# Kernel tuning notes

Measured on AMD Instinct MI355X. Metric: run time of the kernel, lower is better.

Reference implementation:

```python
import jax, jax.numpy as jnp
import numpy as np

T, B, C, H, L = 384, 48, 256, 256, 2


def setup_inputs() -> dict:
    key = jax.random.key(0)
    ks = jax.random.split(key, 8)
    s = 1.0 / np.sqrt(H)  # torch GRUCell uniform(-1/sqrt(H), 1/sqrt(H)) init
    xav = np.sqrt(2.0 / (H + 1))  # xavier_normal_ for the [1,H] skip-gate linear
    return {
        "x": jax.random.normal(ks[0], (T, B, C), jnp.float32),
        "hiddens": jax.random.normal(ks[1], (L, 1, H), jnp.float32),
        "w_ih": jax.random.uniform(ks[2], (L, 3 * H, C), jnp.float32, -s, s),
        "w_hh": jax.random.uniform(ks[3], (L, 3 * H, H), jnp.float32, -s, s),
        "b_ih": jax.random.uniform(ks[4], (L, 3 * H), jnp.float32, -s, s),
        "b_hh": jax.random.uniform(ks[5], (L, 3 * H), jnp.float32, -s, s),
        "lw": jax.random.normal(ks[6], (L, 1, H), jnp.float32) * xav,
        "lb": jnp.ones((L, 1), jnp.float32),  # linear.bias.data.fill_(1)
    }


def _ste(v):
    # straight-through round: forward round, backward identity
    return v + jax.lax.stop_gradient(jnp.round(v) - v)


def reference(x, hiddens, w_ih, w_hh, b_ih, b_hh, lw, lb):
    Tn, Bn, _ = x.shape
    Ln, _, Hn = hiddens.shape
    skip = jnp.zeros((Bn,), dtype=bool)          # carried across layers (as in torch loop)
    du = jnp.zeros((Bn, 1), x.dtype)             # delta_u, carried across layers
    inp = x
    hs, bus = [], []
    for i in range(Ln):
        wi, wh, bi, bh = w_ih[i], w_hh[i], b_ih[i], b_hh[i]
        lwi, lbi = lw[i], lb[i]
        h0 = jnp.broadcast_to(hiddens[i], (Bn, Hn))  # h.repeat(1, bs, 1)
        u0 = jnp.ones((Bn, 1), x.dtype)              # u reset per layer

        def step(carry, x_t):
            h, u, skp, d = carry
            bu = _ste(u)                                  # [B,1]
            # GRUCell: gates order (r, z, n)
            gi = x_t @ wi.T + bi                          # [B,3H]
            gh = h @ wh.T + bh                            # [B,3H]
            i_r, i_z, i_n = jnp.split(gi, 3, axis=1)
            h_r, h_z, h_n = jnp.split(gh, 3, axis=1)
            r = jax.nn.sigmoid(i_r + h_r)
            z = jax.nn.sigmoid(i_z + h_z)
            n = jnp.tanh(i_n + r * h_n)
            cand = (1.0 - z) * n + z * h
            # non-skip branch
            h_ns = cand * bu
            d_ns = jax.nn.sigmoid(h_ns @ lwi.T + lbi)     # [B,1]
            s = skp[:, None]
            new_h = jnp.where(s, h * (1.0 - bu), h_ns)
            new_d = jnp.where(s, d, d_ns)
            new_u = jnp.where(s, jnp.clip(u + d, 0.0, 1.0) * (1.0 - bu), d_ns * bu)
            # n_skips_after = ceil(0.5/new_u) - 1 ; skip if > 0 (non-diff path)
            nsa = jnp.ceil(0.5 / jax.lax.stop_gradient(new_u)) - 1.0
            new_skip = nsa[:, 0] > 0
            return (new_h, new_u, new_skip, new_d), (new_h, bu)

        (h_f, _, skip, du), (ys, bu_seq) = jax.lax.scan(step, (h0, u0, skip, du), inp)
        inp = ys                 # [T,B,H] feeds next layer
        hs.append(h_f)           # final hidden [B,H]
        bus.append(bu_seq)       # [T,B,1]
    out = inp
    hs = jnp.stack(hs, axis=0)                                   # [L,B,H]
    total_u = jnp.concatenate([b[:, :, 0].T for b in bus], 1)    # [B, L*T]
    return (out, hs, total_u)
```

## Files before the change

kernel.cpp:

```cpp
#include <hip/hip_runtime.h>
#include <stdint.h>


#define T_STEPS 384
#define BATCH   48
#define HID     256

__device__ __forceinline__ float sigm_(float x) { return 1.f / (1.f + __expf(-x)); }
__device__ __forceinline__ float tanh_(float x) {
    float ax = fabsf(x);
    float e  = __expf(-2.f * ax);
    float r  = (1.f - e) / (1.f + e);
    return copysignf(r, x);
}

__global__ __launch_bounds__(256, 2) void gemm_nt(const float* __restrict__ X,
                                                  const float* __restrict__ W,
                                                  const float* __restrict__ B,
                                                  float* __restrict__ O)
{
    __shared__ float As[32 * 140];
    __shared__ float Bs[32 * 68];

    const int tid = threadIdx.x;
    const int tx  = tid & 15;
    const int ty  = tid >> 4;
    const int n0  = blockIdx.x * 64;
    const int m0  = blockIdx.y * 128;

    float acc[8][4];
#pragma unroll
    for (int i = 0; i < 8; ++i)
#pragma unroll
        for (int j = 0; j < 4; ++j) acc[i][j] = 0.f;

    const float4 bias4 = *reinterpret_cast<const float4*>(B + n0 + tx * 4);

    for (int kc = 0; kc < 8; ++kc) {
        const int k0 = kc * 32;
        float4 a[4], bb[2];
#pragma unroll
        for (int j = 0; j < 4; ++j) {
            int f = tid + 256 * j, r = f >> 3, cq = f & 7;
            a[j] = *reinterpret_cast<const float4*>(X + (size_t)(m0 + r) * 256 + k0 + cq * 4);
        }
#pragma unroll
        for (int j = 0; j < 2; ++j) {
            int f = tid + 256 * j, r = f >> 3, cq = f & 7;
            bb[j] = *reinterpret_cast<const float4*>(W + (size_t)(n0 + r) * 256 + k0 + cq * 4);
        }
        __syncthreads();
#pragma unroll
        for (int j = 0; j < 4; ++j) {
            int f = tid + 256 * j, r = f >> 3, cq = f & 7;
            As[(cq * 4 + 0) * 140 + r] = a[j].x;
            As[(cq * 4 + 1) * 140 + r] = a[j].y;
            As[(cq * 4 + 2) * 140 + r] = a[j].z;
            As[(cq * 4 + 3) * 140 + r] = a[j].w;
        }
#pragma unroll
        for (int j = 0; j < 2; ++j) {
            int f = tid + 256 * j, r = f >> 3, cq = f & 7;
            Bs[(cq * 4 + 0) * 68 + r] = bb[j].x;
            Bs[(cq * 4 + 1) * 68 + r] = bb[j].y;
            Bs[(cq * 4 + 2) * 68 + r] = bb[j].z;
            Bs[(cq * 4 + 3) * 68 + r] = bb[j].w;
        }
        __syncthreads();
#pragma unroll 8
        for (int kk = 0; kk < 32; ++kk) {
            float4 av0 = *reinterpret_cast<const float4*>(As + kk * 140 + ty * 8);
            float4 av1 = *reinterpret_cast<const float4*>(As + kk * 140 + ty * 8 + 4);
            float4 bv  = *reinterpret_cast<const float4*>(Bs + kk * 68 + tx * 4);
            float am[8] = {av0.x, av0.y, av0.z, av0.w, av1.x, av1.y, av1.z, av1.w};
            float bn[4] = {bv.x, bv.y, bv.z, bv.w};
#pragma unroll
            for (int i = 0; i < 8; ++i)
#pragma unroll
                for (int j = 0; j < 4; ++j) acc[i][j] = fmaf(am[i], bn[j], acc[i][j]);
        }
    }
#pragma unroll
    for (int i = 0; i < 8; ++i) {
        int row = m0 + ty * 8 + i;
        float4 o;
        o.x = acc[i][0] + bias4.x;
        o.y = acc[i][1] + bias4.y;
        o.z = acc[i][2] + bias4.z;
        o.w = acc[i][3] + bias4.w;
        *reinterpret_cast<float4*>(O + (size_t)row * 768 + n0 + tx * 4) = o;
    }
}

__global__ __launch_bounds__(512, 2) void rec_layer(
    const float* __restrict__ GI, float* __restrict__ Yout,
    const float* __restrict__ whh, const float* __restrict__ bhh,
    const float* __restrict__ lwl, const float* __restrict__ lbl,
    const float* __restrict__ hid,
    unsigned long long* XH, unsigned long long* PD,
    float* __restrict__ hsout, float* __restrict__ tuout)
{
    __shared__ float hbuf[2112];
    __shared__ float pdw[2][8];

    const int tid  = threadIdx.x;
    const int lane = tid & 63;
    const int w    = tid >> 6;
    const int g    = lane & 15;
    const int s    = lane >> 4;
    const int b    = blockIdx.x % 48;
    const int p    = blockIdx.x / 48;
    const int q    = 1 - p;
    const int c    = p * 128 + w * 16 + g;

    float4 Wr[16], Wz[16], Wn[16];
    {
        const float4* wr4 = reinterpret_cast<const float4*>(whh + (size_t)c * 256 + s * 64);
        const float4* wz4 = reinterpret_cast<const float4*>(whh + (size_t)(256 + c) * 256 + s * 64);
        const float4* wn4 = reinterpret_cast<const float4*>(whh + (size_t)(512 + c) * 256 + s * 64);
#pragma unroll
        for (int i = 0; i < 16; ++i) { Wr[i] = wr4[i]; Wz[i] = wz4[i]; Wn[i] = wn4[i]; }
    }

    const float bhr = bhh[c], bhz = bhh[256 + c], bhn = bhh[512 + c];
    const float lwc = lwl[c];
    const float lbv = lbl[0];

    if (tid < 256) {
        float v = hid[tid];
        hbuf[tid] = v; hbuf[264 + tid] = v; hbuf[528 + tid] = v; hbuf[792 + tid] = v;
    }
    __syncthreads();

    float u = 1.f, d = 0.f;
    bool  skip = false;
    int   ns = 0;
    int   hp = 0;

    unsigned long long* XHb = XH + b * 512;
    unsigned long long* PDb = PD + b * 4;

    for (int t = 0; t < T_STEPS; ++t) {
        const float bu  = rintf(u);
        const float obu = 1.f - bu;
        const size_t yrow = ((size_t)t * 48 + b) * 256;

        if (skip) {
            float* hb = hbuf + hp * 1056;
            if (s == 0) {
                float hcv = hb[c];
                float nh  = hcv * obu;
                if (bu != 0.f) { hb[c] = nh; hb[264 + c] = nh; hb[528 + c] = nh; hb[792 + c] = nh; }
                Yout[yrow + c] = nh;
                if (t == T_STEPS - 1) hsout[b * 256 + c] = nh;
            }
            if (p == 0 && tid == 0) tuout[b * 768 + t] = bu;
            u    = fminf(fmaxf(u + d, 0.f), 1.f) * obu;
            skip = (u < 0.5f);
            __syncthreads();
        } else {
            const int sl = ns & 1;
            const unsigned int tag = (unsigned int)ns + 1u;
            const size_t gbase = ((size_t)t * 48 + b) * 768 + c;
            const float gir = GI[gbase], giz = GI[gbase + 256], gin = GI[gbase + 512];

            float ar = 0.f, az = 0.f, an = 0.f;
            const float4* h4 = reinterpret_cast<const float4*>(hbuf + hp * 1056 + s * 328);
#pragma unroll
            for (int i = 0; i < 16; ++i) {
                float4 hv = h4[i];
                ar = fmaf(Wr[i].x, hv.x, ar); ar = fmaf(Wr[i].y, hv.y, ar);
                ar = fmaf(Wr[i].z, hv.z, ar); ar = fmaf(Wr[i].w, hv.w, ar);
                az = fmaf(Wz[i].x, hv.x, az); az = fmaf(Wz[i].y, hv.y, az);
                az = fmaf(Wz[i].z, hv.z, az); az = fmaf(Wz[i].w, hv.w, az);
                an = fmaf(Wn[i].x, hv.x, an); an = fmaf(Wn[i].y, hv.y, an);
                an = fmaf(Wn[i].z, hv.z, an); an = fmaf(Wn[i].w, hv.w, an);
            }
            ar += __shfl_xor(ar, 16); ar += __shfl_xor(ar, 32);
            az += __shfl_xor(az, 16); az += __shfl_xor(az, 32);
            an += __shfl_xor(an, 16); an += __shfl_xor(an, 32);

            float hcv = hbuf[hp * 1056 + s * 264 + c];
            float rr  = sigm_(gir + ar + bhr);
            float zz  = sigm_(giz + az + bhz);
            float nn  = tanh_(gin + rr * (an + bhn));
            float nh  = ((1.f - zz) * nn + zz * hcv) * bu;
            float pdv = nh * lwc;

            float* hbn = hbuf + (hp ^ 1) * 1056;
            if (s == 0) {
                hbn[c] = nh; hbn[264 + c] = nh; hbn[528 + c] = nh; hbn[792 + c] = nh;
                Yout[yrow + c] = nh;
                if (t == T_STEPS - 1) hsout[b * 256 + c] = nh;
                unsigned long long pk = ((unsigned long long)tag << 32) |
                                        (unsigned long long)__float_as_uint(nh);
                __hip_atomic_store(XHb + sl * 256 + c, pk, __ATOMIC_RELAXED, __HIP_MEMORY_SCOPE_AGENT);
            }
            pdv += __shfl_xor(pdv, 1);  pdv += __shfl_xor(pdv, 2);  pdv += __shfl_xor(pdv, 4);
            pdv += __shfl_xor(pdv, 8);  pdv += __shfl_xor(pdv, 16); pdv += __shfl_xor(pdv, 32);
            pdv *= 0.25f;
            if (lane == 0) pdw[sl][w] = pdv;
            if (p == 0 && tid == 0) tuout[b * 768 + t] = bu;
            __syncthreads();

            float ownpd = ((pdw[sl][0] + pdw[sl][1]) + (pdw[sl][2] + pdw[sl][3]))
                        + ((pdw[sl][4] + pdw[sl][5]) + (pdw[sl][6] + pdw[sl][7]));
            if (tid == 0) {
                unsigned long long pk = ((unsigned long long)tag << 32) |
                                        (unsigned long long)__float_as_uint(ownpd);
                __hip_atomic_store(PDb + sl * 2 + p, pk, __ATOMIC_RELAXED, __HIP_MEMORY_SCOPE_AGENT);
            }
            if (tid < 128) {
                int qc = q * 128 + tid;
                unsigned long long pk;
                do {
                    pk = __hip_atomic_load(XHb + sl * 256 + qc, __ATOMIC_RELAXED, __HIP_MEMORY_SCOPE_AGENT);
                } while ((unsigned int)(pk >> 32) < tag);
                float v = __uint_as_float((unsigned int)pk);
                hbn[qc] = v; hbn[264 + qc] = v; hbn[528 + qc] = v; hbn[792 + qc] = v;
            }
            unsigned long long pkq;
            do {
                pkq = __hip_atomic_load(PDb + sl * 2 + q, __ATOMIC_RELAXED, __HIP_MEMORY_SCOPE_AGENT);
            } while ((unsigned int)(pkq >> 32) < tag);
            const float pdq = __uint_as_float((unsigned int)pkq);
            __syncthreads();

            float dns = sigm_((ownpd + pdq) + lbv);
            u = dns * bu; d = dns;
            skip = (u < 0.5f);
            ns++; hp ^= 1;
        }
    }
}

extern "C" void kernel_launch(void* const* d_in, const int* in_sizes, int n_in,
                              void* d_out, int out_size, void* d_ws, size_t ws_size,
                              hipStream_t stream)
{
    const float* x   = (const float*)d_in[0];
    const float* hid = (const float*)d_in[1];
    const float* wih = (const float*)d_in[2];
    const float* whh = (const float*)d_in[3];
    const float* bih = (const float*)d_in[4];
    const float* bhh = (const float*)d_in[5];
    const float* lw  = (const float*)d_in[6];
    const float* lb  = (const float*)d_in[7];
    float* out = (float*)d_out;

    float* ws = (float*)d_ws;
    float* GI = ws;
    float* Y0 = GI + (size_t)18432 * 768;
    unsigned long long* XH0 = (unsigned long long*)(Y0 + (size_t)18432 * 256);
    unsigned long long* XH1 = XH0 + 48 * 512;
    unsigned long long* PD0 = XH1 + 48 * 512;
    unsigned long long* PD1 = PD0 + 48 * 4;

    float* OUTy = out;
    float* HS   = out + (size_t)18432 * 256;
    float* TU   = HS + 2 * 48 * 256;

    hipMemsetAsync(XH0, 0, (size_t)(48 * 512 * 2 + 48 * 4 * 2) * sizeof(unsigned long long), stream);

    dim3 ggrid(12, 144), gblk(256);
    gemm_nt<<<ggrid, gblk, 0, stream>>>(x, wih, bih, GI);
    rec_layer<<<96, 512, 0, stream>>>(GI, Y0, whh, bhh, lw, lb, hid, XH0, PD0, HS, TU);
    gemm_nt<<<ggrid, gblk, 0, stream>>>(Y0, wih + 196608, bih + 768, GI);
    rec_layer<<<96, 512, 0, stream>>>(GI, OUTy, whh + 196608, bhh + 768, lw + 256, lb + 1,
                                      hid + 256, XH1, PD1, HS + 12288, TU + 384);
}
```

Baseline: 2.204 ms.

## Overlap next-step recurrent matvec with cross-block hidden exchange and prefetch GI

Splits each thread's W_hh slice into the half matching its own block's hidden columns and the half owned by the partner block. The next step's matvec is computed inside the current step: the local half runs while the partner's hidden values are still arriving, and the partner half runs after the exchange while the skip-gate partial is still in flight. The next timestep's input-gate values are prefetched, and the exchange store is issued earlier. This moves the recurrent dot products off the critical path between steps, at the cost of more complex control flow and carried state across the skip path, where the accumulators are zeroed when bu is nonzero.

```diff
diff --git a/kernel.cpp b/kernel.cpp
--- a/kernel.cpp
+++ b/kernel.cpp
@@ -113,13 +113,24 @@
     const int q    = 1 - p;
     const int c    = p * 128 + w * 16 + g;
 
-    float4 Wr[16], Wz[16], Wn[16];
+    float4 WrO[8], WzO[8], WnO[8], WrP[8], WzP[8], WnP[8];
     {
-        const float4* wr4 = reinterpret_cast<const float4*>(whh + (size_t)c * 256 + s * 64);
-        const float4* wz4 = reinterpret_cast<const float4*>(whh + (size_t)(256 + c) * 256 + s * 64);
-        const float4* wn4 = reinterpret_cast<const float4*>(whh + (size_t)(512 + c) * 256 + s * 64);
-#pragma unroll
-        for (int i = 0; i < 16; ++i) { Wr[i] = wr4[i]; Wz[i] = wz4[i]; Wn[i] = wn4[i]; }
+        const size_t rR = (size_t)c * 256;
+        const size_t rZ = (size_t)(256 + c) * 256;
+        const size_t rN = (size_t)(512 + c) * 256;
+        const int ko = p * 128 + s * 32;
+        const int kq = q * 128 + s * 32;
+        const float4* a = reinterpret_cast<const float4*>(whh + rR + ko);
+        const float4* bv = reinterpret_cast<const float4*>(whh + rZ + ko);
+        const float4* cv = reinterpret_cast<const float4*>(whh + rN + ko);
+        const float4* d4 = reinterpret_cast<const float4*>(whh + rR + kq);
+        const float4* e4 = reinterpret_cast<const float4*>(whh + rZ + kq);
+        const float4* f4 = reinterpret_cast<const float4*>(whh + rN + kq);
+#pragma unroll
+        for (int i = 0; i < 8; ++i) {
+            WrO[i] = a[i];  WzO[i] = bv[i]; WnO[i] = cv[i];
+            WrP[i] = d4[i]; WzP[i] = e4[i]; WnP[i] = f4[i];
+        }
     }
 
     const float bhr = bhh[c], bhz = bhh[256 + c], bhn = bhh[512 + c];
@@ -131,6 +142,42 @@
         hbuf[tid] = v; hbuf[264 + tid] = v; hbuf[528 + tid] = v; hbuf[792 + tid] = v;
     }
     __syncthreads();
+
+    float gir, giz, gin;
+    {
+        const size_t g0 = (size_t)b * 768 + c;
+        gir = GI[g0]; giz = GI[g0 + 256]; gin = GI[g0 + 512];
+    }
+    float sAr, sAz, sAn;
+    {
+        float ar = 0.f, az = 0.f, an = 0.f;
+        const float4* ho = reinterpret_cast<const float4*>(hbuf + s * 264 + p * 128 + s * 32);
+        const float4* hq = reinterpret_cast<const float4*>(hbuf + s * 264 + q * 128 + s * 32);
+#pragma unroll
+        for (int i = 0; i < 8; ++i) {
+            float4 hv = ho[i];
+            ar = fmaf(WrO[i].x, hv.x, ar); ar = fmaf(WrO[i].y, hv.y, ar);
+            ar = fmaf(WrO[i].z, hv.z, ar); ar = fmaf(WrO[i].w, hv.w, ar);
+            az = fmaf(WzO[i].x, hv.x, az); az = fmaf(WzO[i].y, hv.y, az);
+            az = fmaf(WzO[i].z, hv.z, az); az = fmaf(WzO[i].w, hv.w, az);
+            an = fmaf(WnO[i].x, hv.x, an); an = fmaf(WnO[i].y, hv.y, an);
+            an = fmaf(WnO[i].z, hv.z, an); an = fmaf(WnO[i].w, hv.w, an);
+        }
+#pragma unroll
+        for (int i = 0; i < 8; ++i) {
+            float4 hv = hq[i];
+            ar = fmaf(WrP[i].x, hv.x, ar); ar = fmaf(WrP[i].y, hv.y, ar);
+            ar = fmaf(WrP[i].z, hv.z, ar); ar = fmaf(WrP[i].w, hv.w, ar);
+            az = fmaf(WzP[i].x, hv.x, az); az = fmaf(WzP[i].y, hv.y, az);
+            az = fmaf(WzP[i].z, hv.z, az); az = fmaf(WzP[i].w, hv.w, az);
+            an = fmaf(WnP[i].x, hv.x, an); an = fmaf(WnP[i].y, hv.y, an);
+            an = fmaf(WnP[i].z, hv.z, an); an = fmaf(WnP[i].w, hv.w, an);
+        }
+        ar += __shfl_xor(ar, 16); ar += __shfl_xor(ar, 32);
+        az += __shfl_xor(az, 16); az += __shfl_xor(az, 32);
+        an += __shfl_xor(an, 16); an += __shfl_xor(an, 32);
+        sAr = ar; sAz = az; sAn = an;
+    }
 
     float u = 1.f, d = 0.f;
     bool  skip = false;
@@ -144,6 +191,8 @@
         const float bu  = rintf(u);
         const float obu = 1.f - bu;
         const size_t yrow = ((size_t)t * 48 + b) * 256;
+        const int tp = (t < T_STEPS - 1) ? t + 1 : t;
+        const size_t gpb = ((size_t)tp * 48 + b) * 768 + c;
 
         if (skip) {
             float* hb = hbuf + hp * 1056;
@@ -154,47 +203,32 @@
                 Yout[yrow + c] = nh;
                 if (t == T_STEPS - 1) hsout[b * 256 + c] = nh;
             }
+            if (bu != 0.f) { sAr = 0.f; sAz = 0.f; sAn = 0.f; }
             if (p == 0 && tid == 0) tuout[b * 768 + t] = bu;
+            float pr = GI[gpb], pz = GI[gpb + 256], pn = GI[gpb + 512];
             u    = fminf(fmaxf(u + d, 0.f), 1.f) * obu;
             skip = (u < 0.5f);
             __syncthreads();
+            gir = pr; giz = pz; gin = pn;
         } else {
             const int sl = ns & 1;
             const unsigned int tag = (unsigned int)ns + 1u;
-            const size_t gbase = ((size_t)t * 48 + b) * 768 + c;
-            const float gir = GI[gbase], giz = GI[gbase + 256], gin = GI[gbase + 512];
-
-            float ar = 0.f, az = 0.f, an = 0.f;
-            const float4* h4 = reinterpret_cast<const float4*>(hbuf + hp * 1056 + s * 328);
-#pragma unroll
-            for (int i = 0; i < 16; ++i) {
-                float4 hv = h4[i];
-                ar = fmaf(Wr[i].x, hv.x, ar); ar = fmaf(Wr[i].y, hv.y, ar);
-                ar = fmaf(Wr[i].z, hv.z, ar); ar = fmaf(Wr[i].w, hv.w, ar);
-                az = fmaf(Wz[i].x, hv.x, az); az = fmaf(Wz[i].y, hv.y, az);
-                az = fmaf(Wz[i].z, hv.z, az); az = fmaf(Wz[i].w, hv.w, az);
-                an = fmaf(Wn[i].x, hv.x, an); an = fmaf(Wn[i].y, hv.y, an);
-                an = fmaf(Wn[i].z, hv.z, an); an = fmaf(Wn[i].w, hv.w, an);
-            }
-            ar += __shfl_xor(ar, 16); ar += __shfl_xor(ar, 32);
-            az += __shfl_xor(az, 16); az += __shfl_xor(az, 32);
-            an += __shfl_xor(an, 16); an += __shfl_xor(an, 32);
 
             float hcv = hbuf[hp * 1056 + s * 264 + c];
-            float rr  = sigm_(gir + ar + bhr);
-            float zz  = sigm_(giz + az + bhz);
-            float nn  = tanh_(gin + rr * (an + bhn));
-            float nh  = ((1.f - zz) * nn + zz * hcv) * bu;
+            float rr  = sigm_(gir + sAr + bhr);
+            float zz  = sigm_(giz + sAz + bhz);
+            float tn  = tanh_(gin + rr * (sAn + bhn));
+            float nh  = ((1.f - zz) * tn + zz * hcv) * bu;
             float pdv = nh * lwc;
 
             float* hbn = hbuf + (hp ^ 1) * 1056;
             if (s == 0) {
+                unsigned long long pk0 = ((unsigned long long)tag << 32) |
+                                         (unsigned long long)__float_as_uint(nh);
+                __hip_atomic_store(XHb + sl * 256 + c, pk0, __ATOMIC_RELAXED, __HIP_MEMORY_SCOPE_AGENT);
                 hbn[c] = nh; hbn[264 + c] = nh; hbn[528 + c] = nh; hbn[792 + c] = nh;
                 Yout[yrow + c] = nh;
                 if (t == T_STEPS - 1) hsout[b * 256 + c] = nh;
-                unsigned long long pk = ((unsigned long long)tag << 32) |
-                                        (unsigned long long)__float_as_uint(nh);
-                __hip_atomic_store(XHb + sl * 256 + c, pk, __ATOMIC_RELAXED, __HIP_MEMORY_SCOPE_AGENT);
             }
             pdv += __shfl_xor(pdv, 1);  pdv += __shfl_xor(pdv, 2);  pdv += __shfl_xor(pdv, 4);
             pdv += __shfl_xor(pdv, 8);  pdv += __shfl_xor(pdv, 16); pdv += __shfl_xor(pdv, 32);
@@ -206,30 +240,68 @@
             float ownpd = ((pdw[sl][0] + pdw[sl][1]) + (pdw[sl][2] + pdw[sl][3]))
                         + ((pdw[sl][4] + pdw[sl][5]) + (pdw[sl][6] + pdw[sl][7]));
             if (tid == 0) {
-                unsigned long long pk = ((unsigned long long)tag << 32) |
-                                        (unsigned long long)__float_as_uint(ownpd);
-                __hip_atomic_store(PDb + sl * 2 + p, pk, __ATOMIC_RELAXED, __HIP_MEMORY_SCOPE_AGENT);
+                unsigned long long pk0 = ((unsigned long long)tag << 32) |
+                                         (unsigned long long)__float_as_uint(ownpd);
+                __hip_atomic_store(PDb + sl * 2 + p, pk0, __ATOMIC_RELAXED, __HIP_MEMORY_SCOPE_AGENT);
+            }
+
+            unsigned long long pk = 0;
+            if (tid < 128)
+                pk = __hip_atomic_load(XHb + sl * 256 + q * 128 + tid, __ATOMIC_RELAXED, __HIP_MEMORY_SCOPE_AGENT);
+            float pr = GI[gpb], pz = GI[gpb + 256], pn = GI[gpb + 512];
+
+            float ar = 0.f, az = 0.f, an = 0.f;
+            {
+                const float4* ho = reinterpret_cast<const float4*>(hbn + s * 264 + p * 128 + s * 32);
+#pragma unroll
+                for (int i = 0; i < 8; ++i) {
+                    float4 hv = ho[i];
+                    ar = fmaf(WrO[i].x, hv.x, ar); ar = fmaf(WrO[i].y, hv.y, ar);
+                    ar = fmaf(WrO[i].z, hv.z, ar); ar = fmaf(WrO[i].w, hv.w, ar);
+                    az = fmaf(WzO[i].x, hv.x, az); az = fmaf(WzO[i].y, hv.y, az);
+                    az = fmaf(WzO[i].z, hv.z, az); az = fmaf(WzO[i].w, hv.w, az);
+                    an = fmaf(WnO[i].x, hv.x, an); an = fmaf(WnO[i].y, hv.y, an);
+                    an = fmaf(WnO[i].z, hv.z, an); an = fmaf(WnO[i].w, hv.w, an);
+                }
             }
             if (tid < 128) {
+                while ((unsigned int)(pk >> 32) < tag)
+                    pk = __hip_atomic_load(XHb + sl * 256 + q * 128 + tid, __ATOMIC_RELAXED, __HIP_MEMORY_SCOPE_AGENT);
+                float v = __uint_as_float((unsigned int)pk);
                 int qc = q * 128 + tid;
-                unsigned long long pk;
-                do {
-                    pk = __hip_atomic_load(XHb + sl * 256 + qc, __ATOMIC_RELAXED, __HIP_MEMORY_SCOPE_AGENT);
-                } while ((unsigned int)(pk >> 32) < tag);
-                float v = __uint_as_float((unsigned int)pk);
                 hbn[qc] = v; hbn[264 + qc] = v; hbn[528 + qc] = v; hbn[792 + qc] = v;
             }
-            unsigned long long pkq;
-            do {
+            __syncthreads();
+
+            unsigned long long pkq = __hip_atomic_load(PDb + sl * 2 + q, __ATOMIC_RELAXED, __HIP_MEMORY_SCOPE_AGENT);
+
+            {
+                const float4* hq = reinterpret_cast<const float4*>(hbn + s * 264 + q * 128 + s * 32);
+#pragma unroll
+                for (int i = 0; i < 8; ++i) {
+                    float4 hv = hq[i];
+                    ar = fmaf(WrP[i].x, hv.x, ar); ar = fmaf(WrP[i].y, hv.y, ar);
+                    ar = fmaf(WrP[i].z, hv.z, ar); ar = fmaf(WrP[i].w, hv.w, ar);
+                    az = fmaf(WzP[i].x, hv.x, az); az = fmaf(WzP[i].y, hv.y, az);
+                    az = fmaf(WzP[i].z, hv.z, az); az = fmaf(WzP[i].w, hv.w, az);
+                    an = fmaf(WnP[i].x, hv.x, an); an = fmaf(WnP[i].y, hv.y, an);
+                    an = fmaf(WnP[i].z, hv.z, an); an = fmaf(WnP[i].w, hv.w, an);
+                }
+            }
+            ar += __shfl_xor(ar, 16); ar += __shfl_xor(ar, 32);
+            az += __shfl_xor(az, 16); az += __shfl_xor(az, 32);
+            an += __shfl_xor(an, 16); an += __shfl_xor(an, 32);
+            sAr = ar; sAz = az; sAn = an;
+
+            while ((unsigned int)(pkq >> 32) < tag)
                 pkq = __hip_atomic_load(PDb + sl * 2 + q, __ATOMIC_RELAXED, __HIP_MEMORY_SCOPE_AGENT);
-            } while ((unsigned int)(pkq >> 32) < tag);
             const float pdq = __uint_as_float((unsigned int)pkq);
-            __syncthreads();
 
             float dns = sigm_((ownpd + pdq) + lbv);
             u = dns * bu; d = dns;
             skip = (u < 0.5f);
             ns++; hp ^= 1;
+            gir = pr; giz = pz; gin = pn;
         }
     }
 }
```

After: 2.033 ms. -7.8%, faster.
